# Kernel tuning notes

Hardware: AMD Instinct MI355X
Metric: run time of the kernel (lower is better)

The kernel has to match this reference:

```python
import jax, jax.numpy as jnp
import numpy as np

N_NODES = 50000
N_EDGES = 800000
F_DIM = 64
NEG_SLOPE_ATT = 0.2   # GATConv attention LeakyReLU
NEG_SLOPE_ACT = 0.01  # nn.LeakyReLU default between layers


def setup_inputs() -> dict:
    key = jax.random.key(0)
    ks = jax.random.split(key, 10)
    s = 1.0 / np.sqrt(F_DIM)
    return {
        "x": jax.random.normal(ks[0], (N_NODES, F_DIM), jnp.float32),
        "edge_index": jax.random.randint(ks[1], (2, N_EDGES), 0, N_NODES, jnp.int64),
        "W0": jax.random.normal(ks[2], (F_DIM, F_DIM), jnp.float32) * s,
        "a_src0": jax.random.normal(ks[3], (F_DIM,), jnp.float32) * s,
        "a_dst0": jax.random.normal(ks[4], (F_DIM,), jnp.float32) * s,
        "b0": jnp.zeros((F_DIM,), jnp.float32),
        "W1": jax.random.normal(ks[5], (F_DIM, F_DIM), jnp.float32) * s,
        "a_src1": jax.random.normal(ks[6], (F_DIM,), jnp.float32) * s,
        "a_dst1": jax.random.normal(ks[7], (F_DIM,), jnp.float32) * s,
        "b1": jnp.zeros((F_DIM,), jnp.float32),
    }


def _gat_layer(x, src, dst, W, a_src, a_dst, b, n_nodes):
    # x: [N,F]; src/dst: [E'] (self-loops included)
    h = x @ W                                   # [N,F]
    alpha_s = h @ a_src                          # [N]
    alpha_d = h @ a_dst                          # [N]
    e = jax.nn.leaky_relu(alpha_s[src] + alpha_d[dst], NEG_SLOPE_ATT)  # [E']
    # scatter-softmax over incoming edges per destination node
    m = jax.ops.segment_max(e, dst, num_segments=n_nodes)              # [N]
    ex = jnp.exp(e - m[dst])                                           # [E']
    z = jax.ops.segment_sum(ex, dst, num_segments=n_nodes)             # [N]
    alpha = ex / (z[dst] + 1e-16)                                      # [E']
    out = jax.ops.segment_sum(h[src] * alpha[:, None], dst, num_segments=n_nodes)
    return out + b


def reference(x, edge_index, W0, a_src0, a_dst0, b0, W1, a_src1, a_dst1, b1):
    n = x.shape[0]
    loops = jnp.arange(n, dtype=edge_index.dtype)
    src = jnp.concatenate([edge_index[0], loops])  # add_self_loops=True
    dst = jnp.concatenate([edge_index[1], loops])
    h = _gat_layer(x, src, dst, W0, a_src0, a_dst0, b0, n)
    h = jax.nn.leaky_relu(h, NEG_SLOPE_ACT)
    h = _gat_layer(h, src, dst, W1, a_src1, a_dst1, b1, n)
    h = jax.nn.leaky_relu(h, NEG_SLOPE_ACT)
    return h + x  # residual with original input features
```

## Files before the change

### kernel.cpp

```cpp
#include <hip/hip_runtime.h>
#include <hip/hip_fp16.h>
#include <math.h>

#define NNODES 50000
#define NEDGES 800000
#define F      64
#define NB     782
#define CAP    1408
#define LIN_BLOCKS 1563
#define SBLK   256
#define SIT    13
#define SEPB   (256 * SIT)
#define XSP    68

typedef unsigned short u16;
typedef unsigned int   u32;

__device__ __forceinline__ u32 f2bf2(float a, float b) {
    u32 ua = __float_as_uint(a), ub = __float_as_uint(b);
    ua = (ua + 0x7FFFu + ((ua >> 16) & 1u)) >> 16;
    ub = (ub + 0x7FFFu + ((ub >> 16) & 1u)) >> 16;
    return ua | (ub << 16);
}

#define ACC8(ev, hv) \
    a0 = fmaf(ev, __uint_as_float(hv.x << 16),         a0); \
    a1 = fmaf(ev, __uint_as_float(hv.x & 0xFFFF0000u), a1); \
    a2 = fmaf(ev, __uint_as_float(hv.y << 16),         a2); \
    a3 = fmaf(ev, __uint_as_float(hv.y & 0xFFFF0000u), a3); \
    a4 = fmaf(ev, __uint_as_float(hv.z << 16),         a4); \
    a5 = fmaf(ev, __uint_as_float(hv.z & 0xFFFF0000u), a5); \
    a6 = fmaf(ev, __uint_as_float(hv.w << 16),         a6); \
    a7 = fmaf(ev, __uint_as_float(hv.w & 0xFFFF0000u), a7)

struct LinSmem {
    float Ws[F * F];
    float xs[32 * XSP];
    float asv[F], adv[F];
};

__device__ __forceinline__ void linear_body(
    LinSmem& sm,
    const float* __restrict__ x, const float* __restrict__ W,
    const float* __restrict__ a_src, const float* __restrict__ a_dst,
    u16* __restrict__ h16, float* __restrict__ as_, float* __restrict__ ad_,
    int blk)
{
    const int tid = threadIdx.x;
    const int n   = tid >> 3;
    const int c0  = (tid & 7) * 8;
    const int node = blk * 32 + n;
    const bool valid = node < NNODES;

    for (int i = tid * 4; i < F * F; i += 1024)
        *(float4*)&sm.Ws[i] = *(const float4*)&W[i];
    if (tid < F) { sm.asv[tid] = a_src[tid]; sm.adv[tid] = a_dst[tid]; }
    if (valid) {
        const float4 v0 = *(const float4*)&x[(size_t)node * F + c0];
        const float4 v1 = *(const float4*)&x[(size_t)node * F + c0 + 4];
        *(float4*)&sm.xs[n * XSP + c0]     = v0;
        *(float4*)&sm.xs[n * XSP + c0 + 4] = v1;
    }
    __syncthreads();

    float o0=0.f,o1=0.f,o2=0.f,o3=0.f,o4=0.f,o5=0.f,o6=0.f,o7=0.f;
#pragma unroll 8
    for (int k = 0; k < F; ++k) {
        const float xv = sm.xs[n * XSP + k];
        const float4 wa = *(const float4*)&sm.Ws[k * F + c0];
        const float4 wb = *(const float4*)&sm.Ws[k * F + c0 + 4];
        o0 = fmaf(xv, wa.x, o0); o1 = fmaf(xv, wa.y, o1);
        o2 = fmaf(xv, wa.z, o2); o3 = fmaf(xv, wa.w, o3);
        o4 = fmaf(xv, wb.x, o4); o5 = fmaf(xv, wb.y, o5);
        o6 = fmaf(xv, wb.z, o6); o7 = fmaf(xv, wb.w, o7);
    }

    float vs = o0*sm.asv[c0]   + o1*sm.asv[c0+1] + o2*sm.asv[c0+2] + o3*sm.asv[c0+3]
             + o4*sm.asv[c0+4] + o5*sm.asv[c0+5] + o6*sm.asv[c0+6] + o7*sm.asv[c0+7];
    float vd = o0*sm.adv[c0]   + o1*sm.adv[c0+1] + o2*sm.adv[c0+2] + o3*sm.adv[c0+3]
             + o4*sm.adv[c0+4] + o5*sm.adv[c0+5] + o6*sm.adv[c0+6] + o7*sm.adv[c0+7];
    vs += __shfl_xor(vs, 1, 64); vs += __shfl_xor(vs, 2, 64); vs += __shfl_xor(vs, 4, 64);
    vd += __shfl_xor(vd, 1, 64); vd += __shfl_xor(vd, 2, 64); vd += __shfl_xor(vd, 4, 64);

    if (valid) {
        if ((tid & 7) == 0) { as_[node] = vs; ad_[node] = vd; }
        uint4 p;
        p.x = f2bf2(o0, o1); p.y = f2bf2(o2, o3);
        p.z = f2bf2(o4, o5); p.w = f2bf2(o6, o7);
        *(uint4*)&h16[(size_t)node * F + c0] = p;
    }
}

__global__ __launch_bounds__(256) void stage_linear1(
    const float* __restrict__ x, const float* __restrict__ W,
    const float* __restrict__ a_src, const float* __restrict__ a_dst,
    u16* __restrict__ h16, float* __restrict__ as_, float* __restrict__ ad_,
    const int* __restrict__ src, const int* __restrict__ dst,
    int* __restrict__ gcur, u32* __restrict__ stg)
{
    __shared__ LinSmem sm;
    if (blockIdx.x < SBLK) {
        int* cnt   = (int*)&sm;
        int* lbase = cnt + NB;
        for (int i = threadIdx.x; i < NB; i += 256) cnt[i] = 0;
        __syncthreads();
        const int base = blockIdx.x * SEPB;
        u32 pk_[SIT];
        int bp_[SIT];
#pragma unroll
        for (int it = 0; it < SIT; ++it) {
            const int e = base + it * 256 + threadIdx.x;
            if (e < NEDGES) {
                const int s = src[e], d = dst[e];
                pk_[it] = ((u32)(d & 63) << 16) | (u32)s;
                const int b6 = d >> 6;
                const int pos = atomicAdd(&cnt[b6], 1);
                bp_[it] = b6 | (pos << 10);
            } else {
                bp_[it] = -1; pk_[it] = 0;
            }
        }
        __syncthreads();
        for (int i = threadIdx.x; i < NB; i += 256) {
            const int c = cnt[i];
            lbase[i] = c ? (i * CAP + atomicAdd(&gcur[i], c)) : 0;
        }
        __syncthreads();
#pragma unroll
        for (int it = 0; it < SIT; ++it) {
            if (bp_[it] >= 0) {
                const int b6  = bp_[it] & 1023;
                const int pos = bp_[it] >> 10;
                stg[lbase[b6] + pos] = pk_[it];
            }
        }
        return;
    }
    linear_body(sm, x, W, a_src, a_dst, h16, as_, ad_, blockIdx.x - SBLK);
}

template<int MODE>
__global__ __launch_bounds__(512) void gat_agg(
    const int* __restrict__ gcur, const u32* __restrict__ stg,
    const u16* __restrict__ hin,
    const float* __restrict__ as_, const float* __restrict__ ad_,
    const float* __restrict__ bias,
    const float* __restrict__ Wn, const float* __restrict__ an_s,
    const float* __restrict__ an_d,
    u16* __restrict__ hout, float* __restrict__ as_out, float* __restrict__ ad_out,
    const float* __restrict__ resid, float* __restrict__ out)
{
    __shared__ u32  csrE[CAP];
    __shared__ int  cnt[64];
    __shared__ int  rp[64];
    __shared__ float advn[64];
    __shared__ float asnn[64];
    __shared__ float Ws[MODE == 0 ? F * F : 1];
    __shared__ float asv[MODE == 0 ? F : 1], adv[MODE == 0 ? F : 1];
    __shared__ float xs[MODE == 0 ? 64 * XSP : 1];

    const int tid   = threadIdx.x;
    const int b     = blockIdx.x;
    const int nbase = b << 6;
    const int nr    = (NNODES - nbase < 64) ? (NNODES - nbase) : 64;
    const int m     = gcur[b];

    if (tid < 64) {
        cnt[tid]  = 0;
        const bool v = tid < nr;
        advn[tid] = v ? ad_[nbase + tid] : 0.f;
        asnn[tid] = v ? as_[nbase + tid] : 0.f;
    }
    if constexpr (MODE == 0) {
        for (int i = tid * 4; i < F * F; i += 2048)
            *(float4*)&Ws[i] = *(const float4*)&Wn[i];
        if (tid < F) { asv[tid] = an_s[tid]; adv[tid] = an_d[tid]; }
    }
    __syncthreads();

    for (int i = tid; i < m; i += 512)
        atomicAdd(&cnt[stg[b * CAP + i] >> 16], 1);
    __syncthreads();
    if (tid < 64) {
        const int v = cnt[tid];
        int incl = v;
#pragma unroll
        for (int off = 1; off < 64; off <<= 1) {
            const int t = __shfl_up(incl, off, 64);
            if (tid >= off) incl += t;
        }
        rp[tid]  = incl - v;
        cnt[tid] = incl - v;
    }
    __syncthreads();
    for (int i = tid; i < m; i += 512) {
        const u32 pk = stg[b * CAP + i];
        const int d6 = pk >> 16;
        const int s  = pk & 0xFFFFu;
        float r = as_[s] + advn[d6];
        r = (r > 0.f) ? r : 0.2f * r;
        const float ev = __expf(r);
        const int pos = atomicAdd(&cnt[d6], 1);
        csrE[pos] = ((u32)__half_as_ushort(__float2half(ev)) << 16) | (u32)s;
    }
    __syncthreads();

    const int n   = tid >> 3;
    const int l   = tid & 7;
    const int beg = rp[n];
    const int deg = cnt[n] - rp[n];

    float a0=0.f,a1=0.f,a2=0.f,a3=0.f,a4=0.f,a5=0.f,a6=0.f,a7=0.f;
    float z = 0.f;
    const int nfull = deg & ~3;
    int i = 0;
    for (; i < nfull; i += 4) {
        const u32 p1 = csrE[beg + i];
        const u32 p2 = csrE[beg + i + 1];
        const u32 p3 = csrE[beg + i + 2];
        const u32 p4 = csrE[beg + i + 3];
        const uint4 h1 = ((const uint4*)(hin + (size_t)(p1 & 0xFFFFu) * F))[l];
        const uint4 h2 = ((const uint4*)(hin + (size_t)(p2 & 0xFFFFu) * F))[l];
        const uint4 h3 = ((const uint4*)(hin + (size_t)(p3 & 0xFFFFu) * F))[l];
        const uint4 h4 = ((const uint4*)(hin + (size_t)(p4 & 0xFFFFu) * F))[l];
        const float e1 = __half2float(__ushort_as_half((u16)(p1 >> 16)));
        const float e2 = __half2float(__ushort_as_half((u16)(p2 >> 16)));
        const float e3 = __half2float(__ushort_as_half((u16)(p3 >> 16)));
        const float e4 = __half2float(__ushort_as_half((u16)(p4 >> 16)));
        z += (e1 + e2) + (e3 + e4);
        ACC8(e1, h1); ACC8(e2, h2); ACC8(e3, h3); ACC8(e4, h4);
    }
    if (i < deg) {
        const int j2 = (i + 1 < deg) ? (i + 1) : i;
        const int j3 = (i + 2 < deg) ? (i + 2) : i;
        const u32 p1 = csrE[beg + i];
        const u32 p2 = csrE[beg + j2];
        const u32 p3 = csrE[beg + j3];
        const uint4 h1 = ((const uint4*)(hin + (size_t)(p1 & 0xFFFFu) * F))[l];
        const uint4 h2 = ((const uint4*)(hin + (size_t)(p2 & 0xFFFFu) * F))[l];
        const uint4 h3 = ((const uint4*)(hin + (size_t)(p3 & 0xFFFFu) * F))[l];
        const float e1 = __half2float(__ushort_as_half((u16)(p1 >> 16)));
        const float e2 = (i + 1 < deg) ? __half2float(__ushort_as_half((u16)(p2 >> 16))) : 0.f;
        const float e3 = (i + 2 < deg) ? __half2float(__ushort_as_half((u16)(p3 >> 16))) : 0.f;
        z += e1 + e2 + e3;
        ACC8(e1, h1); ACC8(e2, h2); ACC8(e3, h3);
    }
    if (n < nr) {
        float r = asnn[n] + advn[n];
        r = (r > 0.f) ? r : 0.2f * r;
        const float ev = __expf(r);
        const uint4 hs = ((const uint4*)(hin + (size_t)(nbase + n) * F))[l];
        z += ev;
        ACC8(ev, hs);
    }

    const float inv = 1.f / (z + 1e-16f);
    const float4 b0v = *(const float4*)&bias[l * 8];
    const float4 b1v = *(const float4*)&bias[l * 8 + 4];
    float v0 = a0 * inv + b0v.x, v1 = a1 * inv + b0v.y;
    float v2 = a2 * inv + b0v.z, v3 = a3 * inv + b0v.w;
    float v4 = a4 * inv + b1v.x, v5 = a5 * inv + b1v.y;
    float v6 = a6 * inv + b1v.z, v7 = a7 * inv + b1v.w;
    v0 = (v0 > 0.f) ? v0 : 0.01f * v0;  v1 = (v1 > 0.f) ? v1 : 0.01f * v1;
    v2 = (v2 > 0.f) ? v2 : 0.01f * v2;  v3 = (v3 > 0.f) ? v3 : 0.01f * v3;
    v4 = (v4 > 0.f) ? v4 : 0.01f * v4;  v5 = (v5 > 0.f) ? v5 : 0.01f * v5;
    v6 = (v6 > 0.f) ? v6 : 0.01f * v6;  v7 = (v7 > 0.f) ? v7 : 0.01f * v7;

    if constexpr (MODE == 0) {
        {
            float4 w0; w0.x = v0; w0.y = v1; w0.z = v2; w0.w = v3;
            float4 w1; w1.x = v4; w1.y = v5; w1.z = v6; w1.w = v7;
            const int xb = n * XSP + l * 8;
            *(float4*)&xs[xb]     = w0;
            *(float4*)&xs[xb + 4] = w1;
        }
        __syncthreads();

        const int nb2 = tid >> 3;
        const int c0  = (tid & 7) * 8;
        float o0=0.f,o1=0.f,o2=0.f,o3=0.f,o4=0.f,o5=0.f,o6=0.f,o7=0.f;
#pragma unroll 8
        for (int k = 0; k < F; ++k) {
            const float xv = xs[nb2 * XSP + k];
            const float4 wa = *(const float4*)&Ws[k * F + c0];
            const float4 wb = *(const float4*)&Ws[k * F + c0 + 4];
            o0 = fmaf(xv, wa.x, o0); o1 = fmaf(xv, wa.y, o1);
            o2 = fmaf(xv, wa.z, o2); o3 = fmaf(xv, wa.w, o3);
            o4 = fmaf(xv, wb.x, o4); o5 = fmaf(xv, wb.y, o5);
            o6 = fmaf(xv, wb.z, o6); o7 = fmaf(xv, wb.w, o7);
        }
        float vs = o0*asv[c0]   + o1*asv[c0+1] + o2*asv[c0+2] + o3*asv[c0+3]
                 + o4*asv[c0+4] + o5*asv[c0+5] + o6*asv[c0+6] + o7*asv[c0+7];
        float vd = o0*adv[c0]   + o1*adv[c0+1] + o2*adv[c0+2] + o3*adv[c0+3]
                 + o4*adv[c0+4] + o5*adv[c0+5] + o6*adv[c0+6] + o7*adv[c0+7];
        vs += __shfl_xor(vs, 1, 64); vs += __shfl_xor(vs, 2, 64); vs += __shfl_xor(vs, 4, 64);
        vd += __shfl_xor(vd, 1, 64); vd += __shfl_xor(vd, 2, 64); vd += __shfl_xor(vd, 4, 64);
        if (nb2 < nr) {
            const int node2 = nbase + nb2;
            if ((tid & 7) == 0) { as_out[node2] = vs; ad_out[node2] = vd; }
            uint4 p;
            p.x = f2bf2(o0, o1); p.y = f2bf2(o2, o3);
            p.z = f2bf2(o4, o5); p.w = f2bf2(o6, o7);
            *(uint4*)&hout[(size_t)node2 * F + c0] = p;
        }
    } else {
        if (n < nr) {
            const int node = nbase + n;
            const float4 r0 = *(const float4*)(resid + (size_t)node * F + l * 8);
            const float4 r1 = *(const float4*)(resid + (size_t)node * F + l * 8 + 4);
            float4 o0, o1;
            o0.x = v0 + r0.x; o0.y = v1 + r0.y; o0.z = v2 + r0.z; o0.w = v3 + r0.w;
            o1.x = v4 + r1.x; o1.y = v5 + r1.y; o1.z = v6 + r1.z; o1.w = v7 + r1.w;
            *(float4*)(out + (size_t)node * F + l * 8)     = o0;
            *(float4*)(out + (size_t)node * F + l * 8 + 4) = o1;
        }
    }
}

extern "C" void kernel_launch(void* const* d_in, const int* in_sizes, int n_in,
                              void* d_out, int out_size, void* d_ws, size_t ws_size,
                              hipStream_t stream)
{
    const float* x   = (const float*)d_in[0];
    const int*   ei  = (const int*)  d_in[1];
    const float* W0  = (const float*)d_in[2];
    const float* as0 = (const float*)d_in[3];
    const float* ad0 = (const float*)d_in[4];
    const float* b0  = (const float*)d_in[5];
    const float* W1  = (const float*)d_in[6];
    const float* as1 = (const float*)d_in[7];
    const float* ad1 = (const float*)d_in[8];
    const float* b1  = (const float*)d_in[9];
    float* out = (float*)d_out;

    const int* src = ei;
    const int* dst = ei + NEDGES;

    char* ws = (char*)d_ws;
    u16*   h16    = (u16*)ws;   ws += (size_t)NNODES * F * 2;
    u16*   h2_16  = (u16*)ws;   ws += (size_t)NNODES * F * 2;
    float* as_    = (float*)ws; ws += (size_t)NNODES * 4;
    float* ad_    = (float*)ws; ws += (size_t)NNODES * 4;
    float* as2    = (float*)ws; ws += (size_t)NNODES * 4;
    float* ad2    = (float*)ws; ws += (size_t)NNODES * 4;
    int*   gcur   = (int*)ws;   ws += (size_t)NB * 4;
    u32*   stg    = (u32*)ws;   ws += (size_t)NB * CAP * 4;

    hipMemsetAsync(gcur, 0, (size_t)NB * 4, stream);
    stage_linear1<<<SBLK + LIN_BLOCKS, 256, 0, stream>>>(
        x, W0, as0, ad0, h16, as_, ad_, src, dst, gcur, stg);

    gat_agg<0><<<NB, 512, 0, stream>>>(
        gcur, stg, h16, as_, ad_, b0,
        W1, as1, ad1, h2_16, as2, ad2, nullptr, nullptr);
    gat_agg<1><<<NB, 512, 0, stream>>>(
        gcur, stg, h2_16, as2, ad2, b1,
        nullptr, nullptr, nullptr, nullptr, nullptr, nullptr, x, out);
}
```

Before: 168.3 us.

## Persist per-bucket CSR order from layer-0 aggregation for reuse in layer 1

Layer-0 aggregation now writes its locally sorted edge order back into the staging buffer and records per-node row offset and degree, so the layer-1 kernel skips the counting pass, prefix scan and atomic scatter and simply recomputes edge weights in place. The binning stage switches from caching packed edges in registers to a two-pass count-then-scatter that rereads the edge lists. Layer-0 keeps its staging entries in registers across the scan (three per thread) instead of reloading them. The cost is extra global writes in layer 0 and a second read of src/dst in the binning stage, against less atomic and sync work in layer 1.

```diff
diff --git a/kernel.cpp b/kernel.cpp
--- a/kernel.cpp
+++ b/kernel.cpp
@@ -100,38 +100,27 @@
 {
     __shared__ LinSmem sm;
     if (blockIdx.x < SBLK) {
-        int* cnt   = (int*)&sm;
-        int* lbase = cnt + NB;
+        int* cnt  = (int*)&sm;
+        int* lcur = cnt + NB;
         for (int i = threadIdx.x; i < NB; i += 256) cnt[i] = 0;
         __syncthreads();
         const int base = blockIdx.x * SEPB;
-        u32 pk_[SIT];
-        int bp_[SIT];
+#pragma unroll
+        for (int it = 0; it < SIT; ++it) {
+            const int e = base + it * 256 + threadIdx.x;
+            if (e < NEDGES) atomicAdd(&cnt[dst[e] >> 6], 1);
+        }
+        __syncthreads();
+        for (int i = threadIdx.x; i < NB; i += 256)
+            lcur[i] = cnt[i] ? (i * CAP + atomicAdd(&gcur[i], cnt[i])) : 0;
+        __syncthreads();
 #pragma unroll
         for (int it = 0; it < SIT; ++it) {
             const int e = base + it * 256 + threadIdx.x;
             if (e < NEDGES) {
                 const int s = src[e], d = dst[e];
-                pk_[it] = ((u32)(d & 63) << 16) | (u32)s;
-                const int b6 = d >> 6;
-                const int pos = atomicAdd(&cnt[b6], 1);
-                bp_[it] = b6 | (pos << 10);
-            } else {
-                bp_[it] = -1; pk_[it] = 0;
-            }
-        }
-        __syncthreads();
-        for (int i = threadIdx.x; i < NB; i += 256) {
-            const int c = cnt[i];
-            lbase[i] = c ? (i * CAP + atomicAdd(&gcur[i], c)) : 0;
-        }
-        __syncthreads();
-#pragma unroll
-        for (int it = 0; it < SIT; ++it) {
-            if (bp_[it] >= 0) {
-                const int b6  = bp_[it] & 1023;
-                const int pos = bp_[it] >> 10;
-                stg[lbase[b6] + pos] = pk_[it];
+                const int p = atomicAdd(&lcur[d >> 6], 1);
+                stg[p] = ((u32)(d & 63) << 16) | (u32)s;
             }
         }
         return;
@@ -139,25 +128,25 @@
     linear_body(sm, x, W, a_src, a_dst, h16, as_, ad_, blockIdx.x - SBLK);
 }
 
-template<int MODE>
-__global__ __launch_bounds__(512) void gat_agg(
-    const int* __restrict__ gcur, const u32* __restrict__ stg,
+#define BITER 3
+__global__ __launch_bounds__(512) void gat_agg0(
+    const int* __restrict__ gcur, u32* __restrict__ stg,
     const u16* __restrict__ hin,
     const float* __restrict__ as_, const float* __restrict__ ad_,
     const float* __restrict__ bias,
     const float* __restrict__ Wn, const float* __restrict__ an_s,
     const float* __restrict__ an_d,
     u16* __restrict__ hout, float* __restrict__ as_out, float* __restrict__ ad_out,
-    const float* __restrict__ resid, float* __restrict__ out)
+    u32* __restrict__ rp32)
 {
     __shared__ u32  csrE[CAP];
     __shared__ int  cnt[64];
     __shared__ int  rp[64];
     __shared__ float advn[64];
     __shared__ float asnn[64];
-    __shared__ float Ws[MODE == 0 ? F * F : 1];
-    __shared__ float asv[MODE == 0 ? F : 1], adv[MODE == 0 ? F : 1];
-    __shared__ float xs[MODE == 0 ? 64 * XSP : 1];
+    __shared__ float Ws[F * F];
+    __shared__ float asv[F], adv[F];
+    __shared__ float xs[64 * XSP];
 
     const int tid   = threadIdx.x;
     const int b     = blockIdx.x;
@@ -171,15 +160,21 @@
         advn[tid] = v ? ad_[nbase + tid] : 0.f;
         asnn[tid] = v ? as_[nbase + tid] : 0.f;
     }
-    if constexpr (MODE == 0) {
-        for (int i = tid * 4; i < F * F; i += 2048)
-            *(float4*)&Ws[i] = *(const float4*)&Wn[i];
-        if (tid < F) { asv[tid] = an_s[tid]; adv[tid] = an_d[tid]; }
-    }
-    __syncthreads();
-
-    for (int i = tid; i < m; i += 512)
-        atomicAdd(&cnt[stg[b * CAP + i] >> 16], 1);
+    for (int i = tid * 4; i < F * F; i += 2048)
+        *(float4*)&Ws[i] = *(const float4*)&Wn[i];
+    if (tid < F) { asv[tid] = an_s[tid]; adv[tid] = an_d[tid]; }
+    __syncthreads();
+
+    u32 pk_[BITER]; int po_[BITER];
+#pragma unroll
+    for (int it = 0; it < BITER; ++it) {
+        const int i = tid + it * 512;
+        if (i < m) {
+            const u32 pk = stg[b * CAP + i];
+            pk_[it] = pk;
+            po_[it] = atomicAdd(&cnt[pk >> 16], 1);
+        } else po_[it] = -1;
+    }
     __syncthreads();
     if (tid < 64) {
         const int v = cnt[tid];
@@ -189,26 +184,30 @@
             const int t = __shfl_up(incl, off, 64);
             if (tid >= off) incl += t;
         }
-        rp[tid]  = incl - v;
-        cnt[tid] = incl - v;
-    }
-    __syncthreads();
-    for (int i = tid; i < m; i += 512) {
-        const u32 pk = stg[b * CAP + i];
-        const int d6 = pk >> 16;
-        const int s  = pk & 0xFFFFu;
-        float r = as_[s] + advn[d6];
-        r = (r > 0.f) ? r : 0.2f * r;
-        const float ev = __expf(r);
-        const int pos = atomicAdd(&cnt[d6], 1);
-        csrE[pos] = ((u32)__half_as_ushort(__float2half(ev)) << 16) | (u32)s;
+        rp[tid] = incl - v;
+        if (tid < nr) rp32[nbase + tid] = (u32)(incl - v) | ((u32)v << 12);
+    }
+    __syncthreads();
+#pragma unroll
+    for (int it = 0; it < BITER; ++it) {
+        if (po_[it] >= 0) {
+            const u32 pk = pk_[it];
+            const int d6 = pk >> 16;
+            const int s  = pk & 0xFFFFu;
+            float r = as_[s] + advn[d6];
+            r = (r > 0.f) ? r : 0.2f * r;
+            const float ev = __expf(r);
+            const int idx = rp[d6] + po_[it];
+            csrE[idx] = ((u32)__half_as_ushort(__float2half(ev)) << 16) | (u32)s;
+            stg[b * CAP + idx] = pk;
+        }
     }
     __syncthreads();
 
     const int n   = tid >> 3;
     const int l   = tid & 7;
     const int beg = rp[n];
-    const int deg = cnt[n] - rp[n];
+    const int deg = cnt[n];
 
     float a0=0.f,a1=0.f,a2=0.f,a3=0.f,a4=0.f,a5=0.f,a6=0.f,a7=0.f;
     float z = 0.f;
@@ -266,54 +265,153 @@
     v4 = (v4 > 0.f) ? v4 : 0.01f * v4;  v5 = (v5 > 0.f) ? v5 : 0.01f * v5;
     v6 = (v6 > 0.f) ? v6 : 0.01f * v6;  v7 = (v7 > 0.f) ? v7 : 0.01f * v7;
 
-    if constexpr (MODE == 0) {
-        {
-            float4 w0; w0.x = v0; w0.y = v1; w0.z = v2; w0.w = v3;
-            float4 w1; w1.x = v4; w1.y = v5; w1.z = v6; w1.w = v7;
-            const int xb = n * XSP + l * 8;
-            *(float4*)&xs[xb]     = w0;
-            *(float4*)&xs[xb + 4] = w1;
-        }
-        __syncthreads();
-
-        const int nb2 = tid >> 3;
-        const int c0  = (tid & 7) * 8;
-        float o0=0.f,o1=0.f,o2=0.f,o3=0.f,o4=0.f,o5=0.f,o6=0.f,o7=0.f;
+    {
+        float4 w0; w0.x = v0; w0.y = v1; w0.z = v2; w0.w = v3;
+        float4 w1; w1.x = v4; w1.y = v5; w1.z = v6; w1.w = v7;
+        const int xb = n * XSP + l * 8;
+        *(float4*)&xs[xb]     = w0;
+        *(float4*)&xs[xb + 4] = w1;
+    }
+    __syncthreads();
+
+    const int nb2 = tid >> 3;
+    const int c0  = (tid & 7) * 8;
+    float o0=0.f,o1=0.f,o2=0.f,o3=0.f,o4=0.f,o5=0.f,o6=0.f,o7=0.f;
 #pragma unroll 8
-        for (int k = 0; k < F; ++k) {
-            const float xv = xs[nb2 * XSP + k];
-            const float4 wa = *(const float4*)&Ws[k * F + c0];
-            const float4 wb = *(const float4*)&Ws[k * F + c0 + 4];
-            o0 = fmaf(xv, wa.x, o0); o1 = fmaf(xv, wa.y, o1);
-            o2 = fmaf(xv, wa.z, o2); o3 = fmaf(xv, wa.w, o3);
-            o4 = fmaf(xv, wb.x, o4); o5 = fmaf(xv, wb.y, o5);
-            o6 = fmaf(xv, wb.z, o6); o7 = fmaf(xv, wb.w, o7);
-        }
-        float vs = o0*asv[c0]   + o1*asv[c0+1] + o2*asv[c0+2] + o3*asv[c0+3]
-                 + o4*asv[c0+4] + o5*asv[c0+5] + o6*asv[c0+6] + o7*asv[c0+7];
-        float vd = o0*adv[c0]   + o1*adv[c0+1] + o2*adv[c0+2] + o3*adv[c0+3]
-                 + o4*adv[c0+4] + o5*adv[c0+5] + o6*adv[c0+6] + o7*adv[c0+7];
-        vs += __shfl_xor(vs, 1, 64); vs += __shfl_xor(vs, 2, 64); vs += __shfl_xor(vs, 4, 64);
-        vd += __shfl_xor(vd, 1, 64); vd += __shfl_xor(vd, 2, 64); vd += __shfl_xor(vd, 4, 64);
-        if (nb2 < nr) {
-            const int node2 = nbase + nb2;
-            if ((tid & 7) == 0) { as_out[node2] = vs; ad_out[node2] = vd; }
-            uint4 p;
-            p.x = f2bf2(o0, o1); p.y = f2bf2(o2, o3);
-            p.z = f2bf2(o4, o5); p.w = f2bf2(o6, o7);
-            *(uint4*)&hout[(size_t)node2 * F + c0] = p;
-        }
-    } else {
-        if (n < nr) {
-            const int node = nbase + n;
-            const float4 r0 = *(const float4*)(resid + (size_t)node * F + l * 8);
-            const float4 r1 = *(const float4*)(resid + (size_t)node * F + l * 8 + 4);
-            float4 o0, o1;
-            o0.x = v0 + r0.x; o0.y = v1 + r0.y; o0.z = v2 + r0.z; o0.w = v3 + r0.w;
-            o1.x = v4 + r1.x; o1.y = v5 + r1.y; o1.z = v6 + r1.z; o1.w = v7 + r1.w;
-            *(float4*)(out + (size_t)node * F + l * 8)     = o0;
-            *(float4*)(out + (size_t)node * F + l * 8 + 4) = o1;
-        }
+    for (int k = 0; k < F; ++k) {
+        const float xv = xs[nb2 * XSP + k];
+        const float4 wa = *(const float4*)&Ws[k * F + c0];
+        const float4 wb = *(const float4*)&Ws[k * F + c0 + 4];
+        o0 = fmaf(xv, wa.x, o0); o1 = fmaf(xv, wa.y, o1);
+        o2 = fmaf(xv, wa.z, o2); o3 = fmaf(xv, wa.w, o3);
+        o4 = fmaf(xv, wb.x, o4); o5 = fmaf(xv, wb.y, o5);
+        o6 = fmaf(xv, wb.z, o6); o7 = fmaf(xv, wb.w, o7);
+    }
+    float vs = o0*asv[c0]   + o1*asv[c0+1] + o2*asv[c0+2] + o3*asv[c0+3]
+             + o4*asv[c0+4] + o5*asv[c0+5] + o6*asv[c0+6] + o7*asv[c0+7];
+    float vd = o0*adv[c0]   + o1*adv[c0+1] + o2*adv[c0+2] + o3*adv[c0+3]
+             + o4*adv[c0+4] + o5*adv[c0+5] + o6*adv[c0+6] + o7*adv[c0+7];
+    vs += __shfl_xor(vs, 1, 64); vs += __shfl_xor(vs, 2, 64); vs += __shfl_xor(vs, 4, 64);
+    vd += __shfl_xor(vd, 1, 64); vd += __shfl_xor(vd, 2, 64); vd += __shfl_xor(vd, 4, 64);
+    if (nb2 < nr) {
+        const int node2 = nbase + nb2;
+        if ((tid & 7) == 0) { as_out[node2] = vs; ad_out[node2] = vd; }
+        uint4 p;
+        p.x = f2bf2(o0, o1); p.y = f2bf2(o2, o3);
+        p.z = f2bf2(o4, o5); p.w = f2bf2(o6, o7);
+        *(uint4*)&hout[(size_t)node2 * F + c0] = p;
+    }
+}
+
+__global__ __launch_bounds__(512) void gat_agg1(
+    const int* __restrict__ gcur, const u32* __restrict__ stg,
+    const u16* __restrict__ hin,
+    const float* __restrict__ as_, const float* __restrict__ ad_,
+    const float* __restrict__ bias, const u32* __restrict__ rp32,
+    const float* __restrict__ resid, float* __restrict__ out)
+{
+    __shared__ u32  csrE[CAP];
+    __shared__ int  rp[64];
+    __shared__ int  dg[64];
+    __shared__ float advn[64];
+    __shared__ float asnn[64];
+
+    const int tid   = threadIdx.x;
+    const int b     = blockIdx.x;
+    const int nbase = b << 6;
+    const int nr    = (NNODES - nbase < 64) ? (NNODES - nbase) : 64;
+    const int m     = gcur[b];
+
+    if (tid < 64) {
+        const bool v = tid < nr;
+        const u32 r = v ? rp32[nbase + tid] : 0;
+        rp[tid] = r & 0xFFFu;
+        dg[tid] = r >> 12;
+        advn[tid] = v ? ad_[nbase + tid] : 0.f;
+        asnn[tid] = v ? as_[nbase + tid] : 0.f;
+    }
+    __syncthreads();
+
+    for (int i = tid; i < m; i += 512) {
+        const u32 pk = stg[b * CAP + i];
+        const int d6 = pk >> 16;
+        const int s  = pk & 0xFFFFu;
+        float r = as_[s] + advn[d6];
+        r = (r > 0.f) ? r : 0.2f * r;
+        const float ev = __expf(r);
+        csrE[i] = ((u32)__half_as_ushort(__float2half(ev)) << 16) | (u32)s;
+    }
+    __syncthreads();
+
+    const int n   = tid >> 3;
+    const int l   = tid & 7;
+    const int beg = rp[n];
+    const int deg = dg[n];
+
+    float a0=0.f,a1=0.f,a2=0.f,a3=0.f,a4=0.f,a5=0.f,a6=0.f,a7=0.f;
+    float z = 0.f;
+    const int nfull = deg & ~3;
+    int i = 0;
+    for (; i < nfull; i += 4) {
+        const u32 p1 = csrE[beg + i];
+        const u32 p2 = csrE[beg + i + 1];
+        const u32 p3 = csrE[beg + i + 2];
+        const u32 p4 = csrE[beg + i + 3];
+        const uint4 h1 = ((const uint4*)(hin + (size_t)(p1 & 0xFFFFu) * F))[l];
+        const uint4 h2 = ((const uint4*)(hin + (size_t)(p2 & 0xFFFFu) * F))[l];
+        const uint4 h3 = ((const uint4*)(hin + (size_t)(p3 & 0xFFFFu) * F))[l];
+        const uint4 h4 = ((const uint4*)(hin + (size_t)(p4 & 0xFFFFu) * F))[l];
+        const float e1 = __half2float(__ushort_as_half((u16)(p1 >> 16)));
+        const float e2 = __half2float(__ushort_as_half((u16)(p2 >> 16)));
+        const float e3 = __half2float(__ushort_as_half((u16)(p3 >> 16)));
+        const float e4 = __half2float(__ushort_as_half((u16)(p4 >> 16)));
+        z += (e1 + e2) + (e3 + e4);
+        ACC8(e1, h1); ACC8(e2, h2); ACC8(e3, h3); ACC8(e4, h4);
+    }
+    if (i < deg) {
+        const int j2 = (i + 1 < deg) ? (i + 1) : i;
+        const int j3 = (i + 2 < deg) ? (i + 2) : i;
+        const u32 p1 = csrE[beg + i];
+        const u32 p2 = csrE[beg + j2];
+        const u32 p3 = csrE[beg + j3];
+        const uint4 h1 = ((const uint4*)(hin + (size_t)(p1 & 0xFFFFu) * F))[l];
+        const uint4 h2 = ((const uint4*)(hin + (size_t)(p2 & 0xFFFFu) * F))[l];
+        const uint4 h3 = ((const uint4*)(hin + (size_t)(p3 & 0xFFFFu) * F))[l];
+        const float e1 = __half2float(__ushort_as_half((u16)(p1 >> 16)));
+        const float e2 = (i + 1 < deg) ? __half2float(__ushort_as_half((u16)(p2 >> 16))) : 0.f;
+        const float e3 = (i + 2 < deg) ? __half2float(__ushort_as_half((u16)(p3 >> 16))) : 0.f;
+        z += e1 + e2 + e3;
+        ACC8(e1, h1); ACC8(e2, h2); ACC8(e3, h3);
+    }
+    if (n < nr) {
+        float r = asnn[n] + advn[n];
+        r = (r > 0.f) ? r : 0.2f * r;
+        const float ev = __expf(r);
+        const uint4 hs = ((const uint4*)(hin + (size_t)(nbase + n) * F))[l];
+        z += ev;
+        ACC8(ev, hs);
+    }
+
+    if (n < nr) {
+        const int node = nbase + n;
+        const float inv = 1.f / (z + 1e-16f);
+        const float4 b0v = *(const float4*)&bias[l * 8];
+        const float4 b1v = *(const float4*)&bias[l * 8 + 4];
+        float v0 = a0 * inv + b0v.x, v1 = a1 * inv + b0v.y;
+        float v2 = a2 * inv + b0v.z, v3 = a3 * inv + b0v.w;
+        float v4 = a4 * inv + b1v.x, v5 = a5 * inv + b1v.y;
+        float v6 = a6 * inv + b1v.z, v7 = a7 * inv + b1v.w;
+        v0 = (v0 > 0.f) ? v0 : 0.01f * v0;  v1 = (v1 > 0.f) ? v1 : 0.01f * v1;
+        v2 = (v2 > 0.f) ? v2 : 0.01f * v2;  v3 = (v3 > 0.f) ? v3 : 0.01f * v3;
+        v4 = (v4 > 0.f) ? v4 : 0.01f * v4;  v5 = (v5 > 0.f) ? v5 : 0.01f * v5;
+        v6 = (v6 > 0.f) ? v6 : 0.01f * v6;  v7 = (v7 > 0.f) ? v7 : 0.01f * v7;
+        const float4 r0 = *(const float4*)(resid + (size_t)node * F + l * 8);
+        const float4 r1 = *(const float4*)(resid + (size_t)node * F + l * 8 + 4);
+        float4 o0, o1;
+        o0.x = v0 + r0.x; o0.y = v1 + r0.y; o0.z = v2 + r0.z; o0.w = v3 + r0.w;
+        o1.x = v4 + r1.x; o1.y = v5 + r1.y; o1.z = v6 + r1.z; o1.w = v7 + r1.w;
+        *(float4*)(out + (size_t)node * F + l * 8)     = o0;
+        *(float4*)(out + (size_t)node * F + l * 8 + 4) = o1;
     }
 }
 
@@ -343,6 +441,7 @@
     float* ad_    = (float*)ws; ws += (size_t)NNODES * 4;
     float* as2    = (float*)ws; ws += (size_t)NNODES * 4;
     float* ad2    = (float*)ws; ws += (size_t)NNODES * 4;
+    u32*   rp32   = (u32*)ws;   ws += (size_t)NNODES * 4;
     int*   gcur   = (int*)ws;   ws += (size_t)NB * 4;
     u32*   stg    = (u32*)ws;   ws += (size_t)NB * CAP * 4;
 
@@ -350,10 +449,9 @@
     stage_linear1<<<SBLK + LIN_BLOCKS, 256, 0, stream>>>(
         x, W0, as0, ad0, h16, as_, ad_, src, dst, gcur, stg);
 
-    gat_agg<0><<<NB, 512, 0, stream>>>(
+    gat_agg0<<<NB, 512, 0, stream>>>(
         gcur, stg, h16, as_, ad_, b0,
-        W1, as1, ad1, h2_16, as2, ad2, nullptr, nullptr);
-    gat_agg<1><<<NB, 512, 0, stream>>>(
-        gcur, stg, h2_16, as2, ad2, b1,
-        nullptr, nullptr, nullptr, nullptr, nullptr, nullptr, x, out);
-}
+        W1, as1, ad1, h2_16, as2, ad2, rp32);
+    gat_agg1<<<NB, 512, 0, stream>>>(
+        gcur, stg, h2_16, as2, ad2, b1, rp32, x, out);
+}
```

After: 166.9 us. About the same (-0.8%).
